# Performance work log

Hardware: AMD Instinct MI355X
Metric: run time of the kernel (lower is better)

## Reference

```python
import jax, jax.numpy as jnp
import numpy as np

NUM_NODES = 100000
EMBED_DIM = 128
HIDDEN = 128
NUM_EDGES = 1600000


def gcn_conv(x, W, b, src, dst, num_nodes):
    """PyG GCNConv: x' = D^{-1/2} (A+I) D^{-1/2} (x W) + b, symmetric norm with self-loops."""
    x = x @ W  # [N, out]
    loops = jnp.arange(num_nodes, dtype=src.dtype)
    s = jnp.concatenate([src, loops])  # sources incl. self-loops
    d = jnp.concatenate([dst, loops])  # targets incl. self-loops
    deg = jax.ops.segment_sum(jnp.ones_like(d, dtype=x.dtype), d, num_segments=num_nodes)
    dis = jnp.where(deg > 0, jax.lax.rsqrt(deg), 0.0)  # deg^{-1/2}, 0 where isolated
    norm = dis[s] * dis[d]  # [E+N]
    msg = x[s] * norm[:, None]  # gather + scale
    out = jax.ops.segment_sum(msg, d, num_segments=num_nodes)  # scatter-add
    return out + b


def setup_inputs() -> dict:
    key = jax.random.key(0)
    k1, k2, k3, k4, k5, k6 = jax.random.split(key, 6)
    edge_index = jax.random.randint(k1, (2, NUM_EDGES), 0, NUM_NODES, dtype=jnp.int64)
    edge_attr = jax.random.normal(k2, (NUM_EDGES,), dtype=jnp.float32)
    emb = jax.random.normal(k3, (NUM_NODES, EMBED_DIM), dtype=jnp.float32) * 0.1
    W1 = jax.random.normal(k4, (EMBED_DIM, HIDDEN), dtype=jnp.float32) * (1.0 / np.sqrt(EMBED_DIM))
    b1 = jnp.zeros((HIDDEN,), dtype=jnp.float32)
    W2 = jax.random.normal(k5, (HIDDEN, HIDDEN), dtype=jnp.float32) * (1.0 / np.sqrt(HIDDEN))
    b2 = jnp.zeros((HIDDEN,), dtype=jnp.float32)
    return {"edge_index": edge_index, "edge_attr": edge_attr, "emb": emb,
            "W1": W1, "b1": b1, "W2": W2, "b2": b2}


def reference(edge_index, edge_attr, emb, W1, b1, W2, b2):
    src, dst = edge_index[0], edge_index[1]
    x = gcn_conv(emb, W1, b1, src, dst, NUM_NODES)
    x = jax.nn.relu(x)
    x = gcn_conv(x, W2, b2, src, dst, NUM_NODES)
    return x
```

## Files before the change

kernel.cpp:

```cpp
#include <hip/hip_runtime.h>

#define EMB 128
#define NBUC 1024
#define NPART 256

typedef __attribute__((ext_vector_type(8))) short short8;
typedef __attribute__((ext_vector_type(4))) float f32x4;

__device__ __forceinline__ unsigned short f2bf(float f) {
    union { float f; unsigned int i; } v; v.f = f;
    unsigned int x = v.i;
    x += 0x7fffu + ((x >> 16) & 1u);
    return (unsigned short)(x >> 16);
}
__device__ __forceinline__ void acc_bf4(uint2 v, float& a0, float& a1, float& a2, float& a3) {
    union { unsigned int i; float f; } t;
    t.i = v.x << 16;          a0 += t.f;
    t.i = v.x & 0xffff0000u;  a1 += t.f;
    t.i = v.y << 16;          a2 += t.f;
    t.i = v.y & 0xffff0000u;  a3 += t.f;
}


__global__ __launch_bounds__(256) void p1_hist(const int* __restrict__ dst,
                                               int* __restrict__ BH, int E, int chunk) {
    __shared__ int h[NBUC];
    for (int i = threadIdx.x; i < NBUC; i += 256) h[i] = 0;
    __syncthreads();
    int s = blockIdx.x * chunk;
    int e = min(E, s + chunk);
    for (int i = s + threadIdx.x; i < e; i += 256)
        atomicAdd(&h[dst[i] >> 7], 1);
    __syncthreads();
    for (int i = threadIdx.x; i < NBUC; i += 256)
        BH[blockIdx.x * NBUC + i] = h[i];
}

__global__ __launch_bounds__(256) void p_tot(const int* __restrict__ BH,
                                             int* __restrict__ tot) {
    int b = blockIdx.x * 256 + threadIdx.x;
    int s = 0;
    for (int blk = 0; blk < NPART; ++blk) s += BH[blk * NBUC + b];
    tot[b] = s;
}

__global__ __launch_bounds__(1024) void p_scan(const int* __restrict__ tot,
                                               int* __restrict__ base, int E) {
    __shared__ int a[NBUC];
    int t = threadIdx.x;
    int v0 = tot[t];
    a[t] = v0;
    __syncthreads();
    for (int off = 1; off < NBUC; off <<= 1) {
        int v = (t >= off) ? a[t - off] : 0;
        __syncthreads();
        a[t] += v;
        __syncthreads();
    }
    base[t] = a[t] - v0;
    if (t == NBUC - 1) base[NBUC] = E;
}

__global__ __launch_bounds__(256) void p_offs(int* __restrict__ BH,
                                              const int* __restrict__ base) {
    int b = blockIdx.x * 256 + threadIdx.x;
    int run = base[b];
    for (int blk = 0; blk < NPART; ++blk) {
        int* p = &BH[blk * NBUC + b];
        int v = *p;
        *p = run;
        run += v;
    }
}

__global__ __launch_bounds__(256) void p2_scatter(const int* __restrict__ src,
                                                  const int* __restrict__ dst,
                                                  const int* __restrict__ BH,
                                                  int* __restrict__ part,
                                                  int E, int chunk) {
    __shared__ int cnt[NBUC];
    for (int i = threadIdx.x; i < NBUC; i += 256)
        cnt[i] = BH[blockIdx.x * NBUC + i];
    __syncthreads();
    int s = blockIdx.x * chunk;
    int e = min(E, s + chunk);
    for (int i = s + threadIdx.x; i < e; i += 256) {
        int d = dst[i];
        int pos = atomicAdd(&cnt[d >> 7], 1);
        part[pos] = src[i] | ((d & 127) << 17);
    }
}

__global__ __launch_bounds__(256) void p3_csr(const int* __restrict__ part,
                                              const int* __restrict__ base,
                                              int* __restrict__ R, int* __restrict__ adj,
                                              float* __restrict__ dis, int N, int E) {
    __shared__ int hist[128];
    __shared__ int sc[128];
    __shared__ int cnt[128];
    int b = blockIdx.x;
    int n0 = b * 128;
    int nn = min(128, N - n0);
    int s = base[b], e = base[b + 1];
    int t = threadIdx.x;

    if (t < 128) hist[t] = 0;
    __syncthreads();
    for (int i = s + t; i < e; i += 256)
        atomicAdd(&hist[part[i] >> 17], 1);
    __syncthreads();

    if (t < 128) sc[t] = hist[t];
    __syncthreads();
    for (int off = 1; off < 128; off <<= 1) {
        int v = 0;
        if (t < 128 && t >= off) v = sc[t - off];
        __syncthreads();
        if (t < 128) sc[t] += v;
        __syncthreads();
    }
    if (t < 128) {
        int excl = sc[t] - hist[t];
        cnt[t] = excl;
        if (t < nn) {
            R[n0 + t] = s + excl;
            dis[n0 + t] = rsqrtf((float)hist[t] + 1.0f);
        }
    }
    if (b == 0 && t == 0) R[N] = E;
    __syncthreads();

    for (int i = s + t; i < e; i += 256) {
        int p = part[i];
        int pos = atomicAdd(&cnt[p >> 17], 1);
        adj[s + pos] = p & 0x1FFFF;
    }
}

__global__ __launch_bounds__(256) void k_prep_w(const float* __restrict__ W,
                                                unsigned short* __restrict__ Ws) {
    int idx = blockIdx.x * 256 + threadIdx.x;
    int k = idx >> 7, n = idx & 127;
    int kk = k >> 5, q = (k >> 3) & 3, j = k & 7;
    int ct = n >> 4, nn = n & 15;
    int didx = ((((kk * 8 + ct) * 4 + q) * 16 + nn) << 3) + j;
    Ws[didx] = f2bf(W[idx]);
}

template <bool XBF16>
__global__ __launch_bounds__(256) void k_gemm_mfma(
    const void* Xv, const unsigned short* __restrict__ Wsw,
    const float* __restrict__ dis, unsigned short* Y, int N)
{
    __shared__ __align__(16) unsigned short lds[16384];

    {
        const uint4* srcp = (const uint4*)Wsw;
        uint4* dstp = (uint4*)lds;
        for (int i = threadIdx.x; i < 2048; i += 256) dstp[i] = srcp[i];
    }
    __syncthreads();

    const int wave = threadIdx.x >> 6;
    const int lane = threadIdx.x & 63;
    const int q = lane >> 4, nn = lane & 15;
    const int row0 = blockIdx.x * 64 + wave * 16;
    const int arow = row0 + nn;
    const int arc = arow < N ? arow : N - 1;

    f32x4 acc[8];
#pragma unroll
    for (int ct = 0; ct < 8; ++ct) acc[ct] = (f32x4){0.f, 0.f, 0.f, 0.f};

#pragma unroll
    for (int kk = 0; kk < 4; ++kk) {
        short8 af;
        if (XBF16) {
            af = *(const short8*)((const unsigned short*)Xv + (size_t)arc * EMB + kk * 32 + q * 8);
        } else {
            const float* xp = (const float*)Xv + (size_t)arc * EMB + kk * 32 + q * 8;
            float4 u0 = *(const float4*)xp;
            float4 u1 = *(const float4*)(xp + 4);
            af[0] = (short)f2bf(u0.x); af[1] = (short)f2bf(u0.y);
            af[2] = (short)f2bf(u0.z); af[3] = (short)f2bf(u0.w);
            af[4] = (short)f2bf(u1.x); af[5] = (short)f2bf(u1.y);
            af[6] = (short)f2bf(u1.z); af[7] = (short)f2bf(u1.w);
        }
#pragma unroll
        for (int ct = 0; ct < 8; ++ct) {
            short8 bf = ((const short8*)lds)[(kk * 8 + ct) * 64 + lane];
            acc[ct] = __builtin_amdgcn_mfma_f32_16x16x32_bf16(af, bf, acc[ct], 0, 0, 0);
        }
    }

    __syncthreads();

    float dv[4];
#pragma unroll
    for (int r = 0; r < 4; ++r) {
        int gm = row0 + q * 4 + r;
        dv[r] = dis[gm < N ? gm : N - 1];
    }
#pragma unroll
    for (int ct = 0; ct < 8; ++ct) {
#pragma unroll
        for (int r = 0; r < 4; ++r) {
            int ml = wave * 16 + q * 4 + r;
            lds[ml * 136 + ct * 16 + nn] = f2bf(acc[ct][r] * dv[r]);
        }
    }
    __syncthreads();

    const int rbase = blockIdx.x * 64;
    for (int i = threadIdx.x; i < 1024; i += 256) {
        int row = i >> 4, off = i & 15;
        int grow = rbase + row;
        if (grow < N) {
            uint4 v = *(const uint4*)(lds + row * 136 + off * 8);
            *((uint4*)(Y + (size_t)grow * EMB) + off) = v;
        }
    }
}

template <bool RELU, bool BF16OUT>
__global__ __launch_bounds__(256) void k_gather_finalize(
    const int* __restrict__ R, const int* __restrict__ adj,
    const unsigned short* __restrict__ Y, const float* __restrict__ dis,
    const float* __restrict__ bias, void* __restrict__ Outv, int N)
{
    int t = blockIdx.x * 256 + threadIdx.x;
    int n = t >> 5;
    if (n >= N) return;
    int j = (t & 31) * 4;

    int rs = R[n], re = R[n + 1];

    float a0 = 0.f, a1 = 0.f, a2 = 0.f, a3 = 0.f;
    uint2 sv = *(const uint2*)(Y + (size_t)n * EMB + j);
    acc_bf4(sv, a0, a1, a2, a3);

    int e = rs;
    for (; e + 3 < re; e += 4) {
        int s0 = adj[e], s1 = adj[e + 1], s2 = adj[e + 2], s3 = adj[e + 3];
        uint2 v0 = *(const uint2*)(Y + (size_t)s0 * EMB + j);
        uint2 v1 = *(const uint2*)(Y + (size_t)s1 * EMB + j);
        uint2 v2 = *(const uint2*)(Y + (size_t)s2 * EMB + j);
        uint2 v3 = *(const uint2*)(Y + (size_t)s3 * EMB + j);
        acc_bf4(v0, a0, a1, a2, a3);
        acc_bf4(v1, a0, a1, a2, a3);
        acc_bf4(v2, a0, a1, a2, a3);
        acc_bf4(v3, a0, a1, a2, a3);
    }
    for (; e < re; ++e) {
        uint2 v0 = *(const uint2*)(Y + (size_t)adj[e] * EMB + j);
        acc_bf4(v0, a0, a1, a2, a3);
    }

    float dv = dis[n];
    float4 b = *(const float4*)(bias + j);
    float o0 = dv * a0 + b.x;
    float o1 = dv * a1 + b.y;
    float o2 = dv * a2 + b.z;
    float o3 = dv * a3 + b.w;
    if (RELU) {
        o0 = fmaxf(o0, 0.f); o1 = fmaxf(o1, 0.f);
        o2 = fmaxf(o2, 0.f); o3 = fmaxf(o3, 0.f);
    }
    if (BF16OUT) {
        ushort4 o = { f2bf(o0), f2bf(o1), f2bf(o2), f2bf(o3) };
        *(ushort4*)((unsigned short*)Outv + (size_t)n * EMB + j) = o;
    } else {
        float4 o = { o0, o1, o2, o3 };
        *(float4*)((float*)Outv + (size_t)n * EMB + j) = o;
    }
}

extern "C" void kernel_launch(void* const* d_in, const int* in_sizes, int n_in,
                              void* d_out, int out_size, void* d_ws, size_t ws_size,
                              hipStream_t stream) {
    const int* ei = (const int*)d_in[0];
    const int E = in_sizes[0] / 2;
    const float* emb = (const float*)d_in[2];
    const int N = in_sizes[2] / EMB;
    const float* W1 = (const float*)d_in[3];
    const float* b1 = (const float*)d_in[4];
    const float* W2 = (const float*)d_in[5];
    const float* b2 = (const float*)d_in[6];
    float* out = (float*)d_out;

    const int* src = ei;
    const int* dstp = ei + E;

    char* w = (char*)d_ws;
    auto take = [&](size_t bytes) { char* p = w; w += (bytes + 511) & ~(size_t)511; return p; };
    float* dis  = (float*)take((size_t)N * 4);
    int*   R    = (int*)  take((size_t)(N + 1) * 4);
    int*   base = (int*)  take((size_t)(NBUC + 1) * 4);
    int*   tot  = (int*)  take((size_t)NBUC * 4);
    int*   adj  = (int*)  take((size_t)E * 4);
    unsigned short* W1s = (unsigned short*)take((size_t)EMB * EMB * 2);
    unsigned short* W2s = (unsigned short*)take((size_t)EMB * EMB * 2);
    unsigned short* Hb  = (unsigned short*)take((size_t)N * EMB * 2);
    int*   part = (int*)Hb;
    int*   BH   = (int*)((char*)Hb + (((size_t)E * 4 + 511) & ~(size_t)511));
    unsigned short* Y1b = (unsigned short*)d_out;

    const int NB = (N + 127) / 128;
    const int chunk = (E + NPART - 1) / NPART;
    const int gM = (N + 63) / 64;
    const int gG = (N * 32 + 255) / 256;

    p1_hist   <<<NPART, 256, 0, stream>>>(dstp, BH, E, chunk);
    p_tot     <<<NBUC / 256, 256, 0, stream>>>(BH, tot);
    p_scan    <<<1, NBUC, 0, stream>>>(tot, base, E);
    p_offs    <<<NBUC / 256, 256, 0, stream>>>(BH, base);
    p2_scatter<<<NPART, 256, 0, stream>>>(src, dstp, BH, part, E, chunk);
    p3_csr    <<<NB, 256, 0, stream>>>(part, base, R, adj, dis, N, E);

    k_prep_w<<<64, 256, 0, stream>>>(W1, W1s);
    k_prep_w<<<64, 256, 0, stream>>>(W2, W2s);

    k_gemm_mfma<false><<<gM, 256, 0, stream>>>(emb, W1s, dis, Y1b, N);
    k_gather_finalize<true, true><<<gG, 256, 0, stream>>>(R, adj, Y1b, dis, b1, Hb, N);

    k_gemm_mfma<true><<<gM, 256, 0, stream>>>(Hb, W2s, dis, Hb, N);
    k_gather_finalize<false, false><<<gG, 256, 0, stream>>>(R, adj, Hb, dis, b2, out, N);
}
```

Before: 343.8 us.

## Segment bucket-offset scans, merge weight prep, use nontemporal adj loads and stores

The per-bucket total and offset passes are split across 8 segments, so 32 blocks run in place of 4 serial 256-step loops, with the scan summing the segment totals. The two weight-prep launches are merged into one. The gather kernel now loads adjacency indices and writes outputs with nontemporal hints to keep the reused Y rows in cache. The changes trade one extra small buffer and some redundant prefix sums for shorter serial chains and fewer launches.

```diff
diff --git a/kernel.cpp b/kernel.cpp
--- a/kernel.cpp
+++ b/kernel.cpp
@@ -3,9 +3,13 @@
 #define EMB 128
 #define NBUC 1024
 #define NPART 256
+#define NSEG 8
+#define SEGLEN (NPART / NSEG)
 
 typedef __attribute__((ext_vector_type(8))) short short8;
 typedef __attribute__((ext_vector_type(4))) float f32x4;
+typedef __attribute__((ext_vector_type(2))) unsigned int uint2v;
+typedef __attribute__((ext_vector_type(4))) float float4v;
 
 __device__ __forceinline__ unsigned short f2bf(float f) {
     union { float f; unsigned int i; } v; v.f = f;
@@ -36,19 +40,24 @@
         BH[blockIdx.x * NBUC + i] = h[i];
 }
 
-__global__ __launch_bounds__(256) void p_tot(const int* __restrict__ BH,
-                                             int* __restrict__ tot) {
-    int b = blockIdx.x * 256 + threadIdx.x;
+__global__ __launch_bounds__(256) void p_segsum(const int* __restrict__ BH,
+                                                int* __restrict__ SS) {
+    int idx = blockIdx.x * 256 + threadIdx.x;
+    int seg = idx >> 10, b = idx & (NBUC - 1);
     int s = 0;
-    for (int blk = 0; blk < NPART; ++blk) s += BH[blk * NBUC + b];
-    tot[b] = s;
-}
-
-__global__ __launch_bounds__(1024) void p_scan(const int* __restrict__ tot,
+#pragma unroll 8
+    for (int k = 0; k < SEGLEN; ++k)
+        s += BH[(seg * SEGLEN + k) * NBUC + b];
+    SS[seg * NBUC + b] = s;
+}
+
+__global__ __launch_bounds__(1024) void p_scan(const int* __restrict__ SS,
                                                int* __restrict__ base, int E) {
     __shared__ int a[NBUC];
     int t = threadIdx.x;
-    int v0 = tot[t];
+    int v0 = 0;
+#pragma unroll 8
+    for (int s = 0; s < NSEG; ++s) v0 += SS[s * NBUC + t];
     a[t] = v0;
     __syncthreads();
     for (int off = 1; off < NBUC; off <<= 1) {
@@ -61,12 +70,16 @@
     if (t == NBUC - 1) base[NBUC] = E;
 }
 
-__global__ __launch_bounds__(256) void p_offs(int* __restrict__ BH,
-                                              const int* __restrict__ base) {
-    int b = blockIdx.x * 256 + threadIdx.x;
+__global__ __launch_bounds__(256) void p_offs2(int* __restrict__ BH,
+                                               const int* __restrict__ SS,
+                                               const int* __restrict__ base) {
+    int idx = blockIdx.x * 256 + threadIdx.x;
+    int seg = idx >> 10, b = idx & (NBUC - 1);
     int run = base[b];
-    for (int blk = 0; blk < NPART; ++blk) {
-        int* p = &BH[blk * NBUC + b];
+    for (int s = 0; s < seg; ++s) run += SS[s * NBUC + b];
+#pragma unroll 4
+    for (int k = 0; k < SEGLEN; ++k) {
+        int* p = &BH[(seg * SEGLEN + k) * NBUC + b];
         int v = *p;
         *p = run;
         run += v;
@@ -137,9 +150,14 @@
     }
 }
 
-__global__ __launch_bounds__(256) void k_prep_w(const float* __restrict__ W,
-                                                unsigned short* __restrict__ Ws) {
-    int idx = blockIdx.x * 256 + threadIdx.x;
+__global__ __launch_bounds__(256) void k_prep_w2(const float* __restrict__ W1,
+                                                 const float* __restrict__ W2,
+                                                 unsigned short* __restrict__ W1s,
+                                                 unsigned short* __restrict__ W2s) {
+    int gid = blockIdx.x * 256 + threadIdx.x;
+    const float* W = (gid < 16384) ? W1 : W2;
+    unsigned short* Ws = (gid < 16384) ? W1s : W2s;
+    int idx = gid & 16383;
     int k = idx >> 7, n = idx & 127;
     int kk = k >> 5, q = (k >> 3) & 3, j = k & 7;
     int ct = n >> 4, nn = n & 15;
@@ -241,7 +259,10 @@
 
     int e = rs;
     for (; e + 3 < re; e += 4) {
-        int s0 = adj[e], s1 = adj[e + 1], s2 = adj[e + 2], s3 = adj[e + 3];
+        int s0 = __builtin_nontemporal_load(adj + e);
+        int s1 = __builtin_nontemporal_load(adj + e + 1);
+        int s2 = __builtin_nontemporal_load(adj + e + 2);
+        int s3 = __builtin_nontemporal_load(adj + e + 3);
         uint2 v0 = *(const uint2*)(Y + (size_t)s0 * EMB + j);
         uint2 v1 = *(const uint2*)(Y + (size_t)s1 * EMB + j);
         uint2 v2 = *(const uint2*)(Y + (size_t)s2 * EMB + j);
@@ -252,7 +273,8 @@
         acc_bf4(v3, a0, a1, a2, a3);
     }
     for (; e < re; ++e) {
-        uint2 v0 = *(const uint2*)(Y + (size_t)adj[e] * EMB + j);
+        int s0 = __builtin_nontemporal_load(adj + e);
+        uint2 v0 = *(const uint2*)(Y + (size_t)s0 * EMB + j);
         acc_bf4(v0, a0, a1, a2, a3);
     }
 
@@ -267,11 +289,15 @@
         o2 = fmaxf(o2, 0.f); o3 = fmaxf(o3, 0.f);
     }
     if (BF16OUT) {
-        ushort4 o = { f2bf(o0), f2bf(o1), f2bf(o2), f2bf(o3) };
-        *(ushort4*)((unsigned short*)Outv + (size_t)n * EMB + j) = o;
+        uint2v pk;
+        pk.x = (unsigned)f2bf(o0) | ((unsigned)f2bf(o1) << 16);
+        pk.y = (unsigned)f2bf(o2) | ((unsigned)f2bf(o3) << 16);
+        __builtin_nontemporal_store(pk,
+            (uint2v*)((unsigned short*)Outv + (size_t)n * EMB + j));
     } else {
-        float4 o = { o0, o1, o2, o3 };
-        *(float4*)((float*)Outv + (size_t)n * EMB + j) = o;
+        float4v o = { o0, o1, o2, o3 };
+        __builtin_nontemporal_store(o,
+            (float4v*)((float*)Outv + (size_t)n * EMB + j));
     }
 }
 
@@ -296,7 +322,7 @@
     float* dis  = (float*)take((size_t)N * 4);
     int*   R    = (int*)  take((size_t)(N + 1) * 4);
     int*   base = (int*)  take((size_t)(NBUC + 1) * 4);
-    int*   tot  = (int*)  take((size_t)NBUC * 4);
+    int*   SS   = (int*)  take((size_t)NSEG * NBUC * 4);
     int*   adj  = (int*)  take((size_t)E * 4);
     unsigned short* W1s = (unsigned short*)take((size_t)EMB * EMB * 2);
     unsigned short* W2s = (unsigned short*)take((size_t)EMB * EMB * 2);
@@ -309,16 +335,16 @@
     const int chunk = (E + NPART - 1) / NPART;
     const int gM = (N + 63) / 64;
     const int gG = (N * 32 + 255) / 256;
+    const int gS = (NSEG * NBUC) / 256;
 
     p1_hist   <<<NPART, 256, 0, stream>>>(dstp, BH, E, chunk);
-    p_tot     <<<NBUC / 256, 256, 0, stream>>>(BH, tot);
-    p_scan    <<<1, NBUC, 0, stream>>>(tot, base, E);
-    p_offs    <<<NBUC / 256, 256, 0, stream>>>(BH, base);
+    p_segsum  <<<gS, 256, 0, stream>>>(BH, SS);
+    p_scan    <<<1, NBUC, 0, stream>>>(SS, base, E);
+    p_offs2   <<<gS, 256, 0, stream>>>(BH, SS, base);
     p2_scatter<<<NPART, 256, 0, stream>>>(src, dstp, BH, part, E, chunk);
     p3_csr    <<<NB, 256, 0, stream>>>(part, base, R, adj, dis, N, E);
 
-    k_prep_w<<<64, 256, 0, stream>>>(W1, W1s);
-    k_prep_w<<<64, 256, 0, stream>>>(W2, W2s);
+    k_prep_w2<<<128, 256, 0, stream>>>(W1, W2, W1s, W2s);
 
     k_gemm_mfma<false><<<gM, 256, 0, stream>>>(emb, W1s, dis, Y1b, N);
     k_gather_finalize<true, true><<<gG, 256, 0, stream>>>(R, adj, Y1b, dis, b1, Hb, N);
```

Result: no change. 348.8 us (+1.5%).
